# Optimization experiments

Hardware: AMD Instinct MI355X
Metric: run time of the kernel (lower is better)

## Reference

```python
import jax, jax.numpy as jnp
import numpy as np

HEADS, HD = 8, 64

def swish(x):
    return x * jax.nn.sigmoid(x)

def layer_norm(x, eps=1e-5):
    mu = jnp.mean(x, axis=-1, keepdims=True)
    var = jnp.var(x, axis=-1, keepdims=True)
    return (x - mu) / jnp.sqrt(var + eps)

def setup_inputs() -> dict:
    key = jax.random.key(0)
    k1, k2, k3 = jax.random.split(key, 3)
    B, L, D = 2, 2048, 512
    x = jax.random.normal(k1, (B, L, D), jnp.float32)
    cnn_w = jax.random.normal(k2, (HEADS * HD * 3, D, 3), jnp.float32) * 0.02
    cnn_b = jnp.zeros((HEADS * HD * 3,), jnp.float32)
    fc_w = jax.random.normal(k3, (D, HEADS * HD), jnp.float32) * 0.02
    fc_b = jnp.zeros((D,), jnp.float32)
    return {"x": x, "cnn_w": cnn_w, "cnn_b": cnn_b, "fc_w": fc_w, "fc_b": fc_b}

def reference(x, cnn_w, cnn_b, fc_w, fc_b):
    B, L, D = x.shape
    # Conv1d(dims -> heads*hd*3, kernel=3, stride=1, pad=1) on channel-first layout
    xt = jnp.transpose(x, (0, 2, 1))  # [B, D, L]
    y = jax.lax.conv_general_dilated(
        xt, cnn_w, window_strides=(1,), padding=[(1, 1)],
        dimension_numbers=("NCH", "OIH", "NCH"),
    ) + cnn_b[None, :, None]  # [B, 3*H*HD, L]
    qkv = swish(y).reshape(B, HEADS, HD * 3, L)
    q, k, v = jnp.split(qkv, 3, axis=-2)  # each [B, H, HD, L]
    # NOTE: original scales by sqrt(length), not sqrt(hd)
    scores = jnp.einsum("bhdw,bhdm->bhwm", q, k) / jnp.sqrt(jnp.float32(L))
    att = jax.nn.softmax(scores, axis=-1)  # [B, H, L, L]
    new_v = jnp.einsum("bhwm,bhdm->bwhd", att, v).reshape(B, L, HEADS * HD)
    m = swish(new_v @ fc_w.T + fc_b)  # [B, L, D]
    return layer_norm(x * 2 + m)
```

## Files before the change

### kernel.cpp

```cpp
#include <hip/hip_runtime.h>
#include <hip/hip_bf16.h>

#define BB 2
#define LL 2048
#define DD 512
#define HH 8
#define HDM 64
#define SCALE 0.022097086912079608f
#define QSCALE 0.03187935766f

typedef __hip_bfloat16 bf16;
typedef unsigned short u16;
typedef __attribute__((ext_vector_type(8))) short short8v;
typedef __attribute__((ext_vector_type(4))) float float4v;

#define XN  2097152
#define WN  2359296
#define BN  1536
#define FWN 262144
#define FBN 512

__device__ __forceinline__ float b2f(u16 u) {
    return __uint_as_float(((unsigned int)u) << 16);
}
__device__ __forceinline__ u16 f2u(float f) {
    bf16 h = __float2bfloat16(f);
    u16 r;
    __builtin_memcpy(&r, &h, 2);
    return r;
}
__device__ __forceinline__ uint4 pack8(const float* f) {
    uint4 p;
    p.x = (unsigned)f2u(f[0]) | ((unsigned)f2u(f[1]) << 16);
    p.y = (unsigned)f2u(f[2]) | ((unsigned)f2u(f[3]) << 16);
    p.z = (unsigned)f2u(f[4]) | ((unsigned)f2u(f[5]) << 16);
    p.w = (unsigned)f2u(f[6]) | ((unsigned)f2u(f[7]) << 16);
    return p;
}

__device__ __forceinline__ void gld_lds16(const u16* g, u16* l) {
    __builtin_amdgcn_global_load_lds(
        (const __attribute__((address_space(1))) unsigned int*)g,
        (__attribute__((address_space(3))) unsigned int*)l, 16, 0, 0);
}

__device__ __forceinline__ int detect_flag(const u16* __restrict__ xraw) {
    int bad = 0;
    int lane = threadIdx.x & 63;
    for (int i = lane; i < 256; i += 64) {
        float v = b2f(xraw[i]);
        if (!(fabsf(v) < 100.f)) bad = 1;
    }
    return (__ballot(bad) != 0ull) ? 1 : 0;
}

__device__ __forceinline__ void conv8(const void* src, u16* dst, size_t i, int flag) {
    if (flag) {
        const float* s = (const float*)src;
        float f[8];
        float4 a = *(const float4*)(s + i);
        float4 b = *(const float4*)(s + i + 4);
        f[0] = a.x; f[1] = a.y; f[2] = a.z; f[3] = a.w;
        f[4] = b.x; f[5] = b.y; f[6] = b.z; f[7] = b.w;
        *(uint4*)(dst + i) = pack8(f);
    } else {
        *(uint4*)(dst + i) = *(const uint4*)((const u16*)src + i);
    }
}

__global__ __launch_bounds__(256) void prep_kernel(
    const void* __restrict__ xsrc, const void* __restrict__ wsrc,
    const void* __restrict__ bsrc, const void* __restrict__ fwsrc,
    const void* __restrict__ fbsrc,
    u16* __restrict__ xp, u16* __restrict__ wt,
    u16* __restrict__ bc, u16* __restrict__ fwc, u16* __restrict__ fbc)
{
    const int flag = detect_flag((const u16*)xsrc);
    const int bid = blockIdx.x;

    if (bid < 1024) {
        int idx = bid * 256 + threadIdx.x;
        if (idx < 256) {
            int b2  = idx >> 7;
            int r2  = (idx >> 6) & 1;
            int c82 = (idx & 63) * 8;
            size_t off = ((size_t)(b2 * 2050 + (r2 ? 2049 : 0))) * 512 + c82;
            uint4 z = {0u, 0u, 0u, 0u};
            *(uint4*)(xp + off) = z;
        }
        int b   = idx / (LL * 64);
        int rem = idx - b * (LL * 64);
        int l   = rem >> 6;
        int c8  = (rem & 63) * 8;
        size_t si = ((size_t)(b * LL + l)) * 512 + c8;
        size_t di = ((size_t)(b * 2050 + l + 1)) * 512 + c8;
        if (flag) {
            const float* s = (const float*)xsrc;
            float f[8];
            float4 a = *(const float4*)(s + si);
            float4 bq = *(const float4*)(s + si + 4);
            f[0] = a.x; f[1] = a.y; f[2] = a.z; f[3] = a.w;
            f[4] = bq.x; f[5] = bq.y; f[6] = bq.z; f[7] = bq.w;
            *(uint4*)(xp + di) = pack8(f);
        } else {
            *(uint4*)(xp + di) = *(const uint4*)((const u16*)xsrc + si);
        }
    } else if (bid < 2176) {
        int idx = (bid - 1024) * 256 + threadIdx.x;
        int i8  = idx & 63;
        int rem = idx >> 6;
        int k   = rem % 3;
        int o   = rem / 3;
        float f[8];
        if (flag) {
            const float* s = (const float*)wsrc;
#pragma unroll
            for (int j = 0; j < 8; ++j) f[j] = s[(size_t)o * 1536 + (i8 * 8 + j) * 3 + k];
        } else {
            const u16* s = (const u16*)wsrc;
#pragma unroll
            for (int j = 0; j < 8; ++j) f[j] = b2f(s[(size_t)o * 1536 + (i8 * 8 + j) * 3 + k]);
        }
        *(uint4*)(wt + (size_t)o * 1536 + k * 512 + i8 * 8) = pack8(f);
    } else {
        int o = (bid - 2176) * 256 + threadIdx.x;
        if (o < BN / 8) {
            conv8(bsrc, bc, (size_t)o * 8, flag);
        } else if (o < BN / 8 + FWN / 8) {
            conv8(fwsrc, fwc, (size_t)(o - BN / 8) * 8, flag);
        } else if (o < BN / 8 + FWN / 8 + FBN / 8) {
            conv8(fbsrc, fbc, (size_t)(o - BN / 8 - FWN / 8) * 8, flag);
        }
    }
}

__global__ __launch_bounds__(256) void conv_mfma_kernel(
    const u16* __restrict__ xp,
    const u16* __restrict__ wt,
    const u16* __restrict__ bias,
    u16* __restrict__ qkbuf,
    u16* __restrict__ vbuf)
{
    __shared__ u16 smem[32768];
    u16* Asb = smem;
    u16* Bsb = smem + 2 * 128 * 64;
#define OTS 140
    u16* OT  = smem;

    const int blk = blockIdx.x;
    const int rt = blk / 12;
    const int ct = blk - rt * 12;
    const int b  = rt >> 4;
    const int l0 = (rt & 15) * 128;
    const int tid  = threadIdx.x;
    const int wave = tid >> 6;
    const int lane = tid & 63;
    const int quad = lane >> 4;
    const int l16  = lane & 15;
    const int e7   = l16 & 7;
    const int wx = wave & 1;
    const int wy = wave >> 1;

    float4v acc[4][4];
#pragma unroll
    for (int mt = 0; mt < 4; ++mt)
#pragma unroll
        for (int nt = 0; nt < 4; ++nt) acc[mt][nt] = (float4v){0.f, 0.f, 0.f, 0.f};

    const int rowW = wave * 32;
    const int lrow = lane >> 3;
    const int g8   = (((lane & 7) ^ lrow)) * 8;
    auto stage = [&](int kc, int buf) {
        const int slab = kc >> 3;
        const int i0   = (kc & 7) * 64;
        const u16* ga = xp + ((size_t)(b * 2050 + l0 + rowW + slab + lrow)) * 512 + i0 + g8;
        const u16* gb = wt + ((size_t)(ct * 128 + rowW + lrow)) * 1536 + kc * 64 + g8;
        u16* la = Asb + (size_t)(buf * 128 + rowW) * 64;
        u16* lb = Bsb + (size_t)(buf * 128 + rowW) * 64;
#pragma unroll
        for (int j = 0; j < 4; ++j) {
            gld_lds16(ga + (size_t)(j * 8) * 512,  la + (j * 8) * 64);
            gld_lds16(gb + (size_t)(j * 8) * 1536, lb + (j * 8) * 64);
        }
    };

    stage(0, 0);

    for (int kc = 0; kc < 24; ++kc) {
        const int cur = kc & 1;
        __syncthreads();

        if (kc < 23) stage(kc + 1, 1 - cur);

#pragma unroll
        for (int half = 0; half < 2; ++half) {
            const int p = ((half * 4 + quad) ^ e7) * 8;
            short8v aF[4], bF[4];
#pragma unroll
            for (int mt = 0; mt < 4; ++mt)
                aF[mt] = *(const short8v*)&Asb[(size_t)(cur * 128 + wy * 64 + mt * 16 + l16) * 64 + p];
#pragma unroll
            for (int nt = 0; nt < 4; ++nt)
                bF[nt] = *(const short8v*)&Bsb[(size_t)(cur * 128 + wx * 64 + nt * 16 + l16) * 64 + p];
#pragma unroll
            for (int mt = 0; mt < 4; ++mt)
#pragma unroll
                for (int nt = 0; nt < 4; ++nt)
                    acc[mt][nt] = __builtin_amdgcn_mfma_f32_16x16x32_bf16(
                        aF[mt], bF[nt], acc[mt][nt], 0, 0, 0);
        }
    }

    __syncthreads();
    {
        const int tloc = (ct * 2 + wx) % 3;
#pragma unroll
        for (int nt = 0; nt < 4; ++nt) {
            int oc = wx * 64 + nt * 16 + l16;
            float bb = b2f(bias[ct * 128 + oc]);
#pragma unroll
            for (int mt = 0; mt < 4; ++mt)
#pragma unroll
                for (int r = 0; r < 4; ++r) {
                    int lr = wy * 64 + mt * 16 + quad * 4 + r;
                    float y = acc[mt][nt][r] + bb;
                    y = y / (1.f + __expf(-y));
                    if (tloc == 0) y *= QSCALE;
                    OT[lr * OTS + oc] = f2u(y);
                }
        }
    }
    __syncthreads();

#pragma unroll
    for (int g = 0; g < 2; ++g) {
        int a  = ct * 2 + g;
        int t  = a % 3;
        int bh = b * HH + a / 3;
        if (t != 2) {
            u16* base = qkbuf + ((size_t)((bh * 2 + t) * LL + l0)) * HDM;
#pragma unroll
            for (int it = 0; it < 4; ++it) {
                int idx = it * 256 + tid;
                int l   = idx >> 3;
                int d8  = (idx & 7) * 8;
                uint4 val = *(const uint4*)&OT[l * OTS + g * 64 + d8];
                *(uint4*)(base + (size_t)l * HDM + d8) = val;
            }
        } else {
            u16* base = vbuf + ((size_t)(bh * HDM)) * LL + l0;
#pragma unroll
            for (int it = 0; it < 4; ++it) {
                int idx = it * 256 + tid;
                int dd  = idx >> 4;
                int l8  = (idx & 15) * 8;
                u16 tmp[8];
#pragma unroll
                for (int j = 0; j < 8; ++j) tmp[j] = OT[(l8 + j) * OTS + g * 64 + dd];
                uint4 val;
                val.x = (unsigned)tmp[0] | ((unsigned)tmp[1] << 16);
                val.y = (unsigned)tmp[2] | ((unsigned)tmp[3] << 16);
                val.z = (unsigned)tmp[4] | ((unsigned)tmp[5] << 16);
                val.w = (unsigned)tmp[6] | ((unsigned)tmp[7] << 16);
                *(uint4*)(base + (size_t)dd * LL + l8) = val;
            }
        }
    }
#undef OTS
}

__global__ __launch_bounds__(256) void attn_mfma_kernel(
    const u16* __restrict__ qk,
    const u16* __restrict__ v,
    u16* __restrict__ newv)
{
    __shared__ u16 kts[2][128][64];
    __shared__ u16 vts[2][64][128];
    __shared__ u16 pts[4][16][76];

    const int blkid = blockIdx.x;
    const int bh = blkid >> 5;
    const int wc = blkid & 31;
    const int b  = bh >> 3;
    const int h  = bh & 7;
    const int tid  = threadIdx.x;
    const int wave = tid >> 6;
    const int lane = tid & 63;
    const int quad = lane >> 4;
    const int l16  = lane & 15;
    const int e7   = l16 & 7;

    const u16* qbase = qk + ((size_t)(bh * 2 + 0)) * LL * HDM;
    const u16* kbase = qk + ((size_t)(bh * 2 + 1)) * LL * HDM;
    const u16* vbase = v + (size_t)bh * HDM * LL;

    const int w0 = wc * 64 + wave * 16;

    short8v qfrag[2];
    qfrag[0] = *(const short8v*)(qbase + (size_t)(w0 + l16) * HDM + quad * 8);
    qfrag[1] = *(const short8v*)(qbase + (size_t)(w0 + l16) * HDM + 32 + quad * 8);

    short8v vones;
    {
        short o1 = (l16 == 0) ? (short)0x3F80 : (short)0;
#pragma unroll
        for (int j = 0; j < 8; ++j) vones[j] = o1;
    }

    float4v oacc[4];
#pragma unroll
    for (int dt = 0; dt < 4; ++dt) oacc[dt] = (float4v){0.f, 0.f, 0.f, 0.f};
    float4v lacc = (float4v){0.f, 0.f, 0.f, 0.f};

    const int rbK   = wave * 32;
    const int lrowK = lane >> 3;
    const int gK    = ((lane & 7) ^ lrowK) * 8;
    const int rbV   = wave * 16;
    const int lrowV = lane >> 4;
    auto stage = [&](int ic, int buf) {
        const int m0 = ic * 128;
#pragma unroll
        for (int j = 0; j < 4; ++j) {
            gld_lds16(kbase + (size_t)(m0 + rbK + j * 8 + lrowK) * HDM + gK,
                      &kts[buf][rbK + j * 8][0]);
            const int vrow = j * 4 + lrowV;
            gld_lds16(vbase + (size_t)(rbV + vrow) * LL + m0 + (((lane & 15) ^ vrow) * 8),
                      &vts[buf][rbV + j * 4][0]);
        }
    };

    stage(0, 0);

    for (int ic = 0; ic < 16; ++ic) {
        const int cur = ic & 1;
        __syncthreads();

        if (ic < 15) stage(ic + 1, 1 - cur);

        float4v s[8];
#pragma unroll
        for (int mt = 0; mt < 8; ++mt) {
            s[mt] = (float4v){0.f, 0.f, 0.f, 0.f};
            short8v b0 = *(const short8v*)&kts[cur][mt * 16 + l16][((quad) ^ e7) * 8];
            s[mt] = __builtin_amdgcn_mfma_f32_16x16x32_bf16(qfrag[0], b0, s[mt], 0, 0, 0);
            short8v b1 = *(const short8v*)&kts[cur][mt * 16 + l16][((quad + 4) ^ e7) * 8];
            s[mt] = __builtin_amdgcn_mfma_f32_16x16x32_bf16(qfrag[1], b1, s[mt], 0, 0, 0);
        }

#pragma unroll
        for (int g = 0; g < 2; ++g) {
#pragma unroll
            for (int mt4 = 0; mt4 < 4; ++mt4)
#pragma unroll
                for (int r = 0; r < 4; ++r)
                    pts[wave][quad * 4 + r][mt4 * 16 + l16] =
                        f2u(__builtin_amdgcn_exp2f(s[g * 4 + mt4][r]));

            short8v pa0 = *(const short8v*)&pts[wave][l16][quad * 8];
            short8v pa1 = *(const short8v*)&pts[wave][l16][32 + quad * 8];

            lacc = __builtin_amdgcn_mfma_f32_16x16x32_bf16(pa0, vones, lacc, 0, 0, 0);
            lacc = __builtin_amdgcn_mfma_f32_16x16x32_bf16(pa1, vones, lacc, 0, 0, 0);

#pragma unroll
            for (int dt = 0; dt < 4; ++dt) {
                short8v v0 = *(const short8v*)&vts[cur][dt * 16 + l16][((g * 8 + quad) ^ l16) * 8];
                oacc[dt] = __builtin_amdgcn_mfma_f32_16x16x32_bf16(pa0, v0, oacc[dt], 0, 0, 0);
                short8v v1 = *(const short8v*)&vts[cur][dt * 16 + l16][((g * 8 + 4 + quad) ^ l16) * 8];
                oacc[dt] = __builtin_amdgcn_mfma_f32_16x16x32_bf16(pa1, v1, oacc[dt], 0, 0, 0);
            }
        }
    }

    float inv[4];
#pragma unroll
    for (int r = 0; r < 4; ++r) {
        float lsum = __shfl(lacc[r], quad * 16);
        inv[r] = 1.f / lsum;
    }
    u16* ob = newv + (size_t)b * LL * 512 + h * 64;
#pragma unroll
    for (int dt = 0; dt < 4; ++dt)
#pragma unroll
        for (int r = 0; r < 4; ++r) {
            int w = w0 + quad * 4 + r;
            ob[(size_t)w * 512 + dt * 16 + l16] = f2u(oacc[dt][r] * inv[r]);
        }
}

__global__ __launch_bounds__(256) void fc_ln_mfma_kernel(
    const u16* __restrict__ newv,
    const u16* __restrict__ fcw,
    const u16* __restrict__ fcb,
    const u16* __restrict__ xp,
    const u16* __restrict__ xraw,
    void* __restrict__ out)
{
    const int flag = detect_flag(xraw);
    const int l0 = blockIdx.x * 16;
    const int tid  = threadIdx.x;
    const int wave = tid >> 6;
    const int lane = tid & 63;
    const int quad = lane >> 4;
    const int l16  = lane & 15;
    const int col0 = wave * 128;

    const int bb_ = l0 >> 11;
    const size_t xbase = ((size_t)(bb_ * 2050 + (l0 & 2047) + 1)) * 512;

    __shared__ float psum[4][16], psq[4][16];

    short8v aF[16];
    const u16* arow = newv + (size_t)(l0 + l16) * 512 + quad * 8;
#pragma unroll
    for (int kc = 0; kc < 16; ++kc)
        aF[kc] = *(const short8v*)(arow + kc * 32);

    float4v acc[8];
#pragma unroll
    for (int nt = 0; nt < 8; ++nt) acc[nt] = (float4v){0.f, 0.f, 0.f, 0.f};

#pragma unroll
    for (int nt = 0; nt < 8; ++nt) {
        const u16* brow = fcw + (size_t)(col0 + nt * 16 + l16) * 512 + quad * 8;
#pragma unroll
        for (int kc = 0; kc < 16; ++kc) {
            short8v bF = *(const short8v*)(brow + kc * 32);
            acc[nt] = __builtin_amdgcn_mfma_f32_16x16x32_bf16(aF[kc], bF, acc[nt], 0, 0, 0);
        }
    }

    float z[8][4];
    float rs[4] = {0.f, 0.f, 0.f, 0.f}, rq[4] = {0.f, 0.f, 0.f, 0.f};
#pragma unroll
    for (int nt = 0; nt < 8; ++nt) {
        int col = col0 + nt * 16 + l16;
        float bb = b2f(fcb[col]);
#pragma unroll
        for (int r = 0; r < 4; ++r) {
            int row = quad * 4 + r;
            float y = acc[nt][r] + bb;
            float sw = y / (1.f + __expf(-y));
            float xv = b2f(xp[xbase + (size_t)row * 512 + col]);
            float zz = xv * 2.f + sw;
            z[nt][r] = zz;
            rs[r] += zz;
            rq[r] += zz * zz;
        }
    }
#pragma unroll
    for (int msk = 1; msk <= 8; msk <<= 1)
#pragma unroll
        for (int r = 0; r < 4; ++r) {
            rs[r] += __shfl_xor(rs[r], msk);
            rq[r] += __shfl_xor(rq[r], msk);
        }
    if (l16 == 0) {
#pragma unroll
        for (int r = 0; r < 4; ++r) {
            psum[wave][quad * 4 + r] = rs[r];
            psq[wave][quad * 4 + r]  = rq[r];
        }
    }
    __syncthreads();

    float mu[4], inv[4];
#pragma unroll
    for (int r = 0; r < 4; ++r) {
        int row = quad * 4 + r;
        float s = psum[0][row] + psum[1][row] + psum[2][row] + psum[3][row];
        float q = psq[0][row] + psq[1][row] + psq[2][row] + psq[3][row];
        float m = s * (1.f / 512.f);
        float var = q * (1.f / 512.f) - m * m;
        mu[r] = m;
        inv[r] = rsqrtf(var + 1e-5f);
    }

#pragma unroll
    for (int nt = 0; nt < 8; ++nt) {
        int col = col0 + nt * 16 + l16;
#pragma unroll
        for (int r = 0; r < 4; ++r) {
            int row = quad * 4 + r;
            float val = (z[nt][r] - mu[r]) * inv[r];
            if (flag) ((float*)out)[(size_t)(l0 + row) * 512 + col] = val;
            else      ((u16*)out)[(size_t)(l0 + row) * 512 + col] = f2u(val);
        }
    }
}

extern "C" void kernel_launch(void* const* d_in, const int* in_sizes, int n_in,
                              void* d_out, int out_size, void* d_ws, size_t ws_size,
                              hipStream_t stream) {
    (void)in_sizes; (void)n_in; (void)out_size; (void)ws_size;

    char* ws = (char*)d_ws;
    u16* xp   = (u16*)(ws + 256);
    u16* wtc  = (u16*)(ws + 4198656);
    u16* bc   = (u16*)(ws + 8917248);
    u16* fwc  = (u16*)(ws + 8920320);
    u16* fbc  = (u16*)(ws + 9444608);
    u16* qkb  = (u16*)(ws + 9445632);
    u16* vb   = (u16*)(ws + 17834240);
    u16* nvc  = (u16*)(ws + 22028544);

    prep_kernel<<<dim3(2305), dim3(256), 0, stream>>>(
        d_in[0], d_in[1], d_in[2], d_in[3], d_in[4],
        xp, wtc, bc, fwc, fbc);

    conv_mfma_kernel<<<dim3(32 * 12), dim3(256), 0, stream>>>(xp, wtc, bc, qkb, vb);
    attn_mfma_kernel<<<dim3(BB * HH * (LL / 64)), dim3(256), 0, stream>>>(qkb, vb, nvc);
    fc_ln_mfma_kernel<<<dim3(256), dim3(256), 0, stream>>>(
        nvc, fwc, fbc, xp, (const u16*)d_in[0], d_out);
}
```

Before: 168.4 us.

## Keep softmax probabilities in registers via transposed MFMA and permuted V layout

Swaps the MFMA operand order so the score tiles come out transposed, letting each lane pack its exp2 probabilities directly into the B operand for the PV and row-sum MFMAs. This removes the per-wave LDS round trip for P (the pts buffer) along with its stores, loads and LDS footprint. To make this work, the QKV kernel writes V with a permuted column order that matches the register layout of P, and the output store becomes vectorized 4-element writes. The risk is correctness: the permutation must exactly match the MFMA register mapping, and it changes the V write pattern to smaller scattered stores.

Measured after the change: 162.4 us. 3.6% less time.

```diff
diff --git a/kernel.cpp b/kernel.cpp
--- a/kernel.cpp
+++ b/kernel.cpp
@@ -253,16 +253,23 @@
             for (int it = 0; it < 4; ++it) {
                 int idx = it * 256 + tid;
                 int dd  = idx >> 4;
-                int l8  = (idx & 15) * 8;
+                int p   = idx & 15;
+                int l8  = p * 8;
                 u16 tmp[8];
 #pragma unroll
                 for (int j = 0; j < 8; ++j) tmp[j] = OT[(l8 + j) * OTS + g * 64 + dd];
-                uint4 val;
-                val.x = (unsigned)tmp[0] | ((unsigned)tmp[1] << 16);
-                val.y = (unsigned)tmp[2] | ((unsigned)tmp[3] << 16);
-                val.z = (unsigned)tmp[4] | ((unsigned)tmp[5] << 16);
-                val.w = (unsigned)tmp[6] | ((unsigned)tmp[7] << 16);
-                *(uint4*)(base + (size_t)dd * LL + l8) = val;
+                int a32 = p >> 2;
+                int pb_ = p & 3;
+                int q2  = (2 * pb_) & 3;
+                int h2  = pb_ >> 1;
+                int n0  = 32 * a32 + 8 * q2 + 4 * h2;
+                uint2 v0, v1;
+                v0.x = (unsigned)tmp[0] | ((unsigned)tmp[1] << 16);
+                v0.y = (unsigned)tmp[2] | ((unsigned)tmp[3] << 16);
+                v1.x = (unsigned)tmp[4] | ((unsigned)tmp[5] << 16);
+                v1.y = (unsigned)tmp[6] | ((unsigned)tmp[7] << 16);
+                *(uint2*)(base + (size_t)dd * LL + n0)     = v0;
+                *(uint2*)(base + (size_t)dd * LL + n0 + 8) = v1;
             }
         }
     }
@@ -276,7 +283,6 @@
 {
     __shared__ u16 kts[2][128][64];
     __shared__ u16 vts[2][64][128];
-    __shared__ u16 pts[4][16][76];
 
     const int blkid = blockIdx.x;
     const int bh = blkid >> 5;
@@ -342,50 +348,51 @@
         for (int mt = 0; mt < 8; ++mt) {
             s[mt] = (float4v){0.f, 0.f, 0.f, 0.f};
             short8v b0 = *(const short8v*)&kts[cur][mt * 16 + l16][((quad) ^ e7) * 8];
-            s[mt] = __builtin_amdgcn_mfma_f32_16x16x32_bf16(qfrag[0], b0, s[mt], 0, 0, 0);
+            s[mt] = __builtin_amdgcn_mfma_f32_16x16x32_bf16(b0, qfrag[0], s[mt], 0, 0, 0);
             short8v b1 = *(const short8v*)&kts[cur][mt * 16 + l16][((quad + 4) ^ e7) * 8];
-            s[mt] = __builtin_amdgcn_mfma_f32_16x16x32_bf16(qfrag[1], b1, s[mt], 0, 0, 0);
-        }
-
-#pragma unroll
-        for (int g = 0; g < 2; ++g) {
-#pragma unroll
-            for (int mt4 = 0; mt4 < 4; ++mt4)
-#pragma unroll
-                for (int r = 0; r < 4; ++r)
-                    pts[wave][quad * 4 + r][mt4 * 16 + l16] =
-                        f2u(__builtin_amdgcn_exp2f(s[g * 4 + mt4][r]));
-
-            short8v pa0 = *(const short8v*)&pts[wave][l16][quad * 8];
-            short8v pa1 = *(const short8v*)&pts[wave][l16][32 + quad * 8];
-
-            lacc = __builtin_amdgcn_mfma_f32_16x16x32_bf16(pa0, vones, lacc, 0, 0, 0);
-            lacc = __builtin_amdgcn_mfma_f32_16x16x32_bf16(pa1, vones, lacc, 0, 0, 0);
+            s[mt] = __builtin_amdgcn_mfma_f32_16x16x32_bf16(b1, qfrag[1], s[mt], 0, 0, 0);
+        }
+
+        unsigned pk[8][2];
+#pragma unroll
+        for (int mt = 0; mt < 8; ++mt) {
+            float p0 = __builtin_amdgcn_exp2f(s[mt][0]);
+            float p1 = __builtin_amdgcn_exp2f(s[mt][1]);
+            float p2 = __builtin_amdgcn_exp2f(s[mt][2]);
+            float p3 = __builtin_amdgcn_exp2f(s[mt][3]);
+            pk[mt][0] = (unsigned)f2u(p0) | ((unsigned)f2u(p1) << 16);
+            pk[mt][1] = (unsigned)f2u(p2) | ((unsigned)f2u(p3) << 16);
+        }
+
+#pragma unroll
+        for (int mu = 0; mu < 4; ++mu) {
+            union { short8v v8; unsigned u[4]; } U;
+            U.u[0] = pk[2 * mu][0];
+            U.u[1] = pk[2 * mu][1];
+            U.u[2] = pk[2 * mu + 1][0];
+            U.u[3] = pk[2 * mu + 1][1];
+            const short8v pb = U.v8;
+
+            lacc = __builtin_amdgcn_mfma_f32_16x16x32_bf16(vones, pb, lacc, 0, 0, 0);
 
 #pragma unroll
             for (int dt = 0; dt < 4; ++dt) {
-                short8v v0 = *(const short8v*)&vts[cur][dt * 16 + l16][((g * 8 + quad) ^ l16) * 8];
-                oacc[dt] = __builtin_amdgcn_mfma_f32_16x16x32_bf16(pa0, v0, oacc[dt], 0, 0, 0);
-                short8v v1 = *(const short8v*)&vts[cur][dt * 16 + l16][((g * 8 + 4 + quad) ^ l16) * 8];
-                oacc[dt] = __builtin_amdgcn_mfma_f32_16x16x32_bf16(pa1, v1, oacc[dt], 0, 0, 0);
+                short8v va = *(const short8v*)&vts[cur][dt * 16 + l16][((4 * mu + quad) ^ l16) * 8];
+                oacc[dt] = __builtin_amdgcn_mfma_f32_16x16x32_bf16(va, pb, oacc[dt], 0, 0, 0);
             }
         }
     }
 
-    float inv[4];
-#pragma unroll
-    for (int r = 0; r < 4; ++r) {
-        float lsum = __shfl(lacc[r], quad * 16);
-        inv[r] = 1.f / lsum;
-    }
+    float lsum = __shfl(lacc[0], l16);
+    float inv = 1.f / lsum;
     u16* ob = newv + (size_t)b * LL * 512 + h * 64;
 #pragma unroll
-    for (int dt = 0; dt < 4; ++dt)
-#pragma unroll
-        for (int r = 0; r < 4; ++r) {
-            int w = w0 + quad * 4 + r;
-            ob[(size_t)w * 512 + dt * 16 + l16] = f2u(oacc[dt][r] * inv[r]);
-        }
+    for (int dt = 0; dt < 4; ++dt) {
+        unsigned lo = (unsigned)f2u(oacc[dt][0] * inv) | ((unsigned)f2u(oacc[dt][1] * inv) << 16);
+        unsigned hi = (unsigned)f2u(oacc[dt][2] * inv) | ((unsigned)f2u(oacc[dt][3] * inv) << 16);
+        uint2 val; val.x = lo; val.y = hi;
+        *(uint2*)(ob + (size_t)(w0 + l16) * 512 + dt * 16 + quad * 4) = val;
+    }
 }
 
 __global__ __launch_bounds__(256) void fc_ln_mfma_kernel(
```
